# Performance work log

Hardware: AMD Instinct MI355X
Metric: run time of the kernel (lower is better)

The kernel has to match this reference:

```python
import jax, jax.numpy as jnp
import numpy as np
from jax import lax

B, C, H, W = 4, 256, 64, 64
EPS = 1e-5  # BatchNorm eps (eval mode)


def _bn(x, g, b, m, v):
    # eval-mode BatchNorm2d over channel dim
    inv = lax.rsqrt(v + EPS)
    return (x - m[None, :, None, None]) * (g * inv)[None, :, None, None] + b[None, :, None, None]


def _conv1x1(x, w, b):
    # w: [O, I]
    return jnp.einsum('oc,bchw->bohw', w, x) + b[None, :, None, None]


def _conv3x3(x, w, b):
    # w: [O, I, 3, 3], padding 'same'
    y = lax.conv_general_dilated(x, w, (1, 1), 'SAME',
                                 dimension_numbers=('NCHW', 'OIHW', 'NCHW'))
    return y + b[None, :, None, None]


def setup_inputs():
    key = jax.random.key(0)
    ks = jax.random.split(key, 12)
    s = 0.05
    Ch = C // 2
    d = {
        'inputs_0': jax.random.normal(ks[0], (B, C, H, W), jnp.float32),
        'inputs_1': jax.random.normal(ks[1], (B, C, H, W), jnp.float32),
        # 1x1 projections (conv0/conv1/conv2): C -> C/2
        'w_q': jax.random.normal(ks[2], (Ch, C), jnp.float32) * s,
        'b_q': jnp.zeros((Ch,), jnp.float32),
        'w_k': jax.random.normal(ks[3], (Ch, C), jnp.float32) * s,
        'b_k': jnp.zeros((Ch,), jnp.float32),
        'w_v': jax.random.normal(ks[4], (Ch, C), jnp.float32) * s,
        'b_v': jnp.zeros((Ch,), jnp.float32),
        # conv3: C/2 -> C (1x1)
        'w_o': jax.random.normal(ks[5], (C, Ch), jnp.float32) * s,
        'b_o': jnp.zeros((C,), jnp.float32),
        # batch_conv0
        'bn0_g': jnp.ones((C,), jnp.float32), 'bn0_b': jnp.zeros((C,), jnp.float32),
        'bn0_m': jnp.zeros((C,), jnp.float32), 'bn0_v': jnp.ones((C,), jnp.float32),
        # conv_block(2C -> C): conv0 3x3
        'cb_w0': jax.random.normal(ks[6], (C, 2 * C, 3, 3), jnp.float32) * s,
        'cb_b0': jnp.zeros((C,), jnp.float32),
        'cb_bn0_g': jnp.ones((C,), jnp.float32), 'cb_bn0_b': jnp.zeros((C,), jnp.float32),
        'cb_bn0_m': jnp.zeros((C,), jnp.float32), 'cb_bn0_v': jnp.ones((C,), jnp.float32),
        # conv_block conv1 3x3: C -> C
        'cb_w1': jax.random.normal(ks[7], (C, C, 3, 3), jnp.float32) * s,
        'cb_b1': jnp.zeros((C,), jnp.float32),
        'cb_bn1_g': jnp.ones((C,), jnp.float32), 'cb_bn1_b': jnp.zeros((C,), jnp.float32),
        'cb_bn1_m': jnp.zeros((C,), jnp.float32), 'cb_bn1_v': jnp.ones((C,), jnp.float32),
    }
    return d


def reference(inputs_0, inputs_1, w_q, b_q, w_k, b_k, w_v, b_v, w_o, b_o,
              bn0_g, bn0_b, bn0_m, bn0_v,
              cb_w0, cb_b0, cb_bn0_g, cb_bn0_b, cb_bn0_m, cb_bn0_v,
              cb_w1, cb_b1, cb_bn1_g, cb_bn1_b, cb_bn1_m, cb_bn1_v):
    b, c, h, w = inputs_0.shape
    ch = c // 2
    n = h * w
    # 1x1 projections
    x1 = _conv1x1(inputs_0, w_q, b_q).reshape(b, ch, n)   # conv0(inputs_0)
    x2 = _conv1x1(inputs_0, w_k, b_k).reshape(b, ch, n)   # conv1(inputs_0)
    x3 = _conv1x1(inputs_1, w_v, b_v).reshape(b, ch, n)   # conv2(inputs_1)
    # spatial cross-attention: [b, n, n] affinity, contraction over channels
    aff = jnp.einsum('bij,bik->bjk', x2, x3)              # [b, n, n]
    aff = jax.nn.softmax(aff, axis=-2)                    # softmax over dim j (rows)
    x0 = jnp.einsum('bij,bjk->bik', x1, aff)              # [b, ch, n]
    x0 = x0.reshape(b, ch, h, w)
    # output projection + BN + GELU (exact erf gelu, matching torch default)
    x0 = jax.nn.gelu(_bn(_conv1x1(x0, w_o, b_o), bn0_g, bn0_b, bn0_m, bn0_v), approximate=False)
    # conv_block on concat
    y = jnp.concatenate([x0, inputs_0], axis=1)           # [b, 2c, h, w]
    y = jax.nn.gelu(_bn(_conv3x3(y, cb_w0, cb_b0), cb_bn0_g, cb_bn0_b, cb_bn0_m, cb_bn0_v), approximate=False)
    y = jax.nn.gelu(_bn(_conv3x3(y, cb_w1, cb_b1), cb_bn1_g, cb_bn1_b, cb_bn1_m, cb_bn1_v), approximate=False)
    # AdaptiveMaxPool2d((1,1)) == global spatial max, then squeeze -> [b, c]
    out = jnp.max(y + x0, axis=(2, 3))
    return out
```

## Files before the change

### kernel.cpp

```cpp
#include <hip/hip_runtime.h>
#include <math.h>

#define B_ 4
#define C_ 256
#define CH_ 128
#define NN 4096

typedef __bf16 bf16x8 __attribute__((ext_vector_type(8)));
typedef float f32x16 __attribute__((ext_vector_type(16)));
typedef unsigned int u32;

__device__ __forceinline__ float gelu_erf(float x) {
    return 0.5f * x * (1.0f + erff(x * 0.7071067811865476f));
}

__device__ __forceinline__ u32 pkbf(float a, float b) {
    union { __bf16 h[2]; u32 u; } x;
    x.h[0] = (__bf16)a; x.h[1] = (__bf16)b;
    return x.u;
}

__global__ __launch_bounds__(256) void nhwc_cast_kernel(
    const float* __restrict__ src, __bf16* __restrict__ dst,
    int colbase, int rowstride)
{
    __shared__ float Lt[64][65];
    const int t = threadIdx.x;
    const int p0 = blockIdx.x * 64;
    const int c0 = blockIdx.y * 64;
    const int b  = blockIdx.z;
#pragma unroll
    for (int i = 0; i < 16; ++i) {
        int idx = t + i * 256;
        int c = idx >> 6, p = idx & 63;
        Lt[c][p] = src[((size_t)(b * 256 + c0 + c)) * 4096 + p0 + p];
    }
    __syncthreads();
#pragma unroll
    for (int i = 0; i < 16; ++i) {
        int idx = t + i * 256;
        int p = idx >> 6, c = idx & 63;
        dst[((size_t)(b * 4096 + p0 + p)) * rowstride + colbase + c0 + c] = (__bf16)Lt[c][p];
    }
}

__global__ __launch_bounds__(256) void wtrans_kernel(
    const float* __restrict__ w0, const float* __restrict__ w1,
    const float* __restrict__ wq, const float* __restrict__ wk,
    const float* __restrict__ wv, const float* __restrict__ wo,
    __bf16* __restrict__ Wt0, __bf16* __restrict__ Wt1,
    __bf16* __restrict__ wqb, __bf16* __restrict__ wkb,
    __bf16* __restrict__ wvb, __bf16* __restrict__ wob)
{
    int id = blockIdx.x * 256 + threadIdx.x;
    if (id < 131072) {
        int o = id >> 9, ci = id & 511;
        const float* s = w0 + (size_t)id * 9;
        const int chunk = ci >> 4, f = o >> 5;
        const int lane = (o & 31) + 32 * ((ci >> 3) & 1);
        const int j = ci & 7;
#pragma unroll
        for (int k = 0; k < 9; ++k)
            Wt0[((size_t)(chunk * 9 + k) * 8 + f) * 512 + lane * 8 + j] = (__bf16)s[k];
    } else if (id < 196608) {
        int id2 = id - 131072;
        int o = id2 >> 8, ci = id2 & 255;
        const float* s = w1 + (size_t)id2 * 9;
        const int chunk = ci >> 4, f = o >> 5;
        const int lane = (o & 31) + 32 * ((ci >> 3) & 1);
        const int j = ci & 7;
#pragma unroll
        for (int k = 0; k < 9; ++k)
            Wt1[((size_t)(chunk * 9 + k) * 8 + f) * 512 + lane * 8 + j] = (__bf16)s[k];
    } else {
        int id3 = id - 196608;
        int sel = id3 >> 15;
        int k = id3 & 32767;
        const float* s = sel == 0 ? wq : sel == 1 ? wk : sel == 2 ? wv : wo;
        __bf16* d = sel == 0 ? wqb : sel == 1 ? wkb : sel == 2 ? wvb : wob;
        d[k] = (__bf16)s[k];
    }
}

__global__ __launch_bounds__(256) void proj_mfma_kernel(
    const __bf16* __restrict__ Xt0,
    const __bf16* __restrict__ Xin1,
    const __bf16* __restrict__ wqb, const __bf16* __restrict__ wkb,
    const __bf16* __restrict__ wvb,
    const float* __restrict__ bq, const float* __restrict__ bk,
    const float* __restrict__ bv,
    __bf16* __restrict__ Vswz, __bf16* __restrict__ Kswz, __bf16* __restrict__ Qswz)
{
    __shared__ __align__(16) __bf16 Vt[4][64][80];
    __shared__ float biasl[128];

    const int t = threadIdx.x;
    const int which = blockIdx.z % 3;
    const int b = blockIdx.z / 3;
    const int p0 = blockIdx.x * 128;

    const __bf16* W = which == 0 ? wqb : which == 1 ? wkb : wvb;
    const float* bias = which == 0 ? bq : which == 1 ? bk : bv;
    const __bf16* src; int stride, colb;
    if (which == 2) { src = Xin1 + (size_t)b * NN * 256; stride = 256; colb = 0; }
    else            { src = Xt0  + (size_t)b * NN * 512; stride = 512; colb = 256; }

    if (t < 128) biasl[t] = bias[t];
    __syncthreads();

    const int lane = t & 63, w = t >> 6;
    const int l31 = lane & 31, hi = lane >> 5;
    const int wo2 = w >> 1, wp2 = w & 1;
    const int ob = wo2 * 64;
    const int pb = p0 + wp2 * 64;

    f32x16 acc[2][2];
#pragma unroll
    for (int i = 0; i < 2; ++i)
#pragma unroll
        for (int j = 0; j < 2; ++j)
#pragma unroll
            for (int e = 0; e < 16; ++e) acc[i][j][e] = 0.f;

#pragma unroll
    for (int kc = 0; kc < 16; ++kc) {
        bf16x8 a0 = *(const bf16x8*)&W[(size_t)(ob + l31) * 256 + hi * 8 + kc * 16];
        bf16x8 a1 = *(const bf16x8*)&W[(size_t)(ob + 32 + l31) * 256 + hi * 8 + kc * 16];
        bf16x8 b0 = *(const bf16x8*)&src[(size_t)(pb + l31) * stride + colb + hi * 8 + kc * 16];
        bf16x8 b1 = *(const bf16x8*)&src[(size_t)(pb + 32 + l31) * stride + colb + hi * 8 + kc * 16];
        acc[0][0] = __builtin_amdgcn_mfma_f32_32x32x16_bf16(a0, b0, acc[0][0], 0, 0, 0);
        acc[0][1] = __builtin_amdgcn_mfma_f32_32x32x16_bf16(a0, b1, acc[0][1], 0, 0, 0);
        acc[1][0] = __builtin_amdgcn_mfma_f32_32x32x16_bf16(a1, b0, acc[1][0], 0, 0, 0);
        acc[1][1] = __builtin_amdgcn_mfma_f32_32x32x16_bf16(a1, b1, acc[1][1], 0, 0, 0);
    }

    if (which) {
        __bf16* dst = (which == 1 ? Kswz : Qswz) + (size_t)b * NN * CH_;
#pragma unroll
        for (int mi = 0; mi < 2; ++mi)
#pragma unroll
            for (int nx = 0; nx < 2; ++nx) {
                const int tile = (pb >> 5) + nx;
#pragma unroll
                for (int q4 = 0; q4 < 4; ++q4) {
                    const int ic = (ob >> 4) + mi * 2 + (q4 >> 1);
                    const int og = ob + mi * 32 + q4 * 8 + hi * 4;
                    __bf16 pk[4];
#pragma unroll
                    for (int j = 0; j < 4; ++j)
                        pk[j] = (__bf16)(acc[mi][nx][q4 * 4 + j] + biasl[og + j]);
                    const size_t el = ((size_t)(tile * 8 + ic) * 64
                                       + l31 + 32 * (q4 & 1)) * 8 + hi * 4;
                    *(uint2*)&dst[el] = *(const uint2*)pk;
                }
            }
    } else {
#pragma unroll
        for (int mi = 0; mi < 2; ++mi)
#pragma unroll
            for (int nx = 0; nx < 2; ++nx) {
                const int ploc = nx * 32 + l31;
#pragma unroll
                for (int q4 = 0; q4 < 4; ++q4) {
                    const int oloc = mi * 32 + q4 * 8 + hi * 4;
#pragma unroll
                    for (int j = 0; j < 4; ++j)
                        Vt[w][oloc + j][ploc] =
                            (__bf16)(acc[mi][nx][q4 * 4 + j] + biasl[ob + oloc + j]);
                }
            }
        __syncthreads();
        __bf16* dst = Vswz + (size_t)b * NN * CH_;
#pragma unroll
        for (int s = 0; s < 8; ++s) {
            const int tl = s >> 2, jc = (s >> 1) & 1, il = s & 1;
            const int tile_g = (pb >> 5) + tl;
            const int icf_g = (ob >> 5) + il;
            const int i_loc = il * 32 + l31;
            const int kk = tl * 32 + jc * 16 + hi * 8;
            uint4 v = *(const uint4*)&Vt[w][i_loc][kk];
            const size_t el = ((size_t)((tile_g * 2 + jc) * 4 + icf_g) * 64 + lane) * 8;
            *(uint4*)&dst[el] = v;
        }
    }
}

__global__ __launch_bounds__(256, 4) void attn_mfma_kernel(
    const __bf16* __restrict__ Qswz, const __bf16* __restrict__ Kswz,
    const __bf16* __restrict__ Vswz,
    __bf16* __restrict__ Opart, float* __restrict__ Mpart, float* __restrict__ Lpart)
{
    __shared__ __bf16 Op[4][128][34];
    __shared__ float Ml[4][32], Ll[4][32];

    const int t = threadIdx.x;
    const int lane = t & 63;
    const int w = t >> 6;
    const int l31 = lane & 31;
    const int hi = lane >> 5;

    const int bid = blockIdx.x;
    const int xcd = bid & 7;
    const int b = xcd >> 1;
    const int local = bid >> 3;
    const int qt = (xcd & 1) * 64 + (local & 63);
    const int half = local >> 6;
    const int q0 = qt * 32;

    const __bf16* Qs = Qswz + (size_t)b * NN * CH_ + (size_t)qt * 4096 + lane * 8;
    bf16x8 qf[8];
#pragma unroll
    for (int ic = 0; ic < 8; ++ic) qf[ic] = *(const bf16x8*)(Qs + ic * 512);

    const __bf16* Ks = Kswz + (size_t)b * NN * CH_ + lane * 8;
    const __bf16* Vs = Vswz + (size_t)b * NN * CH_ + lane * 8;

    f32x16 oacc[4];
#pragma unroll
    for (int i = 0; i < 4; ++i)
#pragma unroll
        for (int e = 0; e < 16; ++e) oacc[i][e] = 0.f;

    float m = -3e38f, lsum = 0.f;
    const int tbase = half * 64 + w * 16;

    for (int jt = 0; jt < 16; ++jt) {
        const int tile = tbase + jt;
        f32x16 s;
#pragma unroll
        for (int e = 0; e < 16; ++e) s[e] = 0.f;
        const __bf16* Kt = Ks + (size_t)tile * 4096;
#pragma unroll
        for (int ic = 0; ic < 8; ++ic) {
            bf16x8 kf = *(const bf16x8*)(Kt + ic * 512);
            s = __builtin_amdgcn_mfma_f32_32x32x16_bf16(kf, qf[ic], s, 0, 0, 0);
        }
        float t8[8];
#pragma unroll
        for (int e = 0; e < 8; ++e) t8[e] = fmaxf(s[e], s[e + 8]);
#pragma unroll
        for (int e = 0; e < 4; ++e) t8[e] = fmaxf(t8[e], t8[e + 4]);
        t8[0] = fmaxf(t8[0], t8[2]); t8[1] = fmaxf(t8[1], t8[3]);
        float mu = fmaxf(t8[0], t8[1]);
        const float pm = fmaxf(mu, __shfl_xor(mu, 32));
        if (!__all(pm <= m + 8.f)) {
            const float mn = fmaxf(m, pm);
            const float al = __expf(m - mn);
            m = mn;
            lsum *= al;
#pragma unroll
            for (int i = 0; i < 4; ++i)
#pragma unroll
                for (int e = 0; e < 16; ++e) oacc[i][e] *= al;
        }
#pragma unroll
        for (int e = 0; e < 16; ++e) s[e] = __expf(s[e] - m);
        float s8[8];
#pragma unroll
        for (int e = 0; e < 8; ++e) s8[e] = s[e] + s[e + 8];
#pragma unroll
        for (int e = 0; e < 4; ++e) s8[e] += s8[e + 4];
        s8[0] += s8[2]; s8[1] += s8[3];
        float su = s8[0] + s8[1];
        lsum += su + __shfl_xor(su, 32);

        const __bf16* Vt = Vs + (size_t)tile * 4096;
        {
            u32 w0 = pkbf(s[0], s[1]), w1 = pkbf(s[2], s[3]);
            u32 w2 = pkbf(s[4], s[5]), w3 = pkbf(s[6], s[7]);
            asm("v_permlane32_swap_b32 %0, %1" : "+v"(w0), "+v"(w2));
            asm("v_permlane32_swap_b32 %0, %1" : "+v"(w1), "+v"(w3));
            union { u32 u4[4]; bf16x8 v; } pB;
            pB.u4[0] = w0; pB.u4[1] = w1; pB.u4[2] = w2; pB.u4[3] = w3;
#pragma unroll
            for (int icf = 0; icf < 4; ++icf) {
                bf16x8 vf = *(const bf16x8*)(Vt + icf * 512);
                oacc[icf] = __builtin_amdgcn_mfma_f32_32x32x16_bf16(vf, pB.v, oacc[icf], 0, 0, 0);
            }
        }
        {
            u32 w0 = pkbf(s[8], s[9]), w1 = pkbf(s[10], s[11]);
            u32 w2 = pkbf(s[12], s[13]), w3 = pkbf(s[14], s[15]);
            asm("v_permlane32_swap_b32 %0, %1" : "+v"(w0), "+v"(w2));
            asm("v_permlane32_swap_b32 %0, %1" : "+v"(w1), "+v"(w3));
            union { u32 u4[4]; bf16x8 v; } pB;
            pB.u4[0] = w0; pB.u4[1] = w1; pB.u4[2] = w2; pB.u4[3] = w3;
#pragma unroll
            for (int icf = 0; icf < 4; ++icf) {
                bf16x8 vf = *(const bf16x8*)(Vt + 2048 + icf * 512);
                oacc[icf] = __builtin_amdgcn_mfma_f32_32x32x16_bf16(vf, pB.v, oacc[icf], 0, 0, 0);
            }
        }
    }

#pragma unroll
    for (int icf = 0; icf < 4; ++icf)
#pragma unroll
        for (int q = 0; q < 16; ++q) {
            const int row = icf * 32 + (q & 3) + 8 * (q >> 2) + 4 * hi;
            Op[w][row][l31] = (__bf16)oacc[icf][q];
        }
    if (hi == 0) { Ml[w][l31] = m; Ll[w][l31] = lsum; }
    __syncthreads();
    {
        const int q = t & 31;
        const int i0g = (t >> 5) * 16;
        const float m0 = Ml[0][q], m1 = Ml[1][q], m2 = Ml[2][q], m3 = Ml[3][q];
        const float ms = fmaxf(fmaxf(m0, m1), fmaxf(m2, m3));
        const float a0 = __expf(m0 - ms), a1 = __expf(m1 - ms);
        const float a2 = __expf(m2 - ms), a3 = __expf(m3 - ms);
        const float den = a0 * Ll[0][q] + a1 * Ll[1][q] + a2 * Ll[2][q] + a3 * Ll[3][q];
        union { __bf16 h[16]; uint4 u4[2]; } pk;
#pragma unroll
        for (int ii = 0; ii < 16; ++ii) {
            const int i = i0g + ii;
            pk.h[ii] = (__bf16)(a0 * (float)Op[0][i][q] + a1 * (float)Op[1][i][q]
                              + a2 * (float)Op[2][i][q] + a3 * (float)Op[3][i][q]);
        }
        const size_t base = ((size_t)((half * 4 + b) * NN) + q0 + q) * CH_ + i0g;
        *(uint4*)&Opart[base] = pk.u4[0];
        *(uint4*)&Opart[base + 8] = pk.u4[1];
        if (t < 32) {
            Mpart[(size_t)(half * 4 + b) * NN + q0 + q] = ms;
            Lpart[(size_t)(half * 4 + b) * NN + q0 + q] = den;
        }
    }
}

__global__ __launch_bounds__(256) void attn_merge_kernel(
    const __bf16* __restrict__ Opart, const float* __restrict__ Mpart,
    const float* __restrict__ Lpart, __bf16* __restrict__ x0)
{
    const int id = blockIdx.x * 256 + threadIdx.x;
    const int qg = id >> 2;
    const int i0 = (id & 3) * 32;
    const int b = qg >> 12, q = qg & 4095;
    const size_t idx0 = (size_t)b * NN + q;
    const size_t idx1 = (size_t)(4 + b) * NN + q;
    const float m0 = Mpart[idx0], m1 = Mpart[idx1];
    const float ms = fmaxf(m0, m1);
    const float a0 = __expf(m0 - ms), a1 = __expf(m1 - ms);
    const float inv = 1.f / (a0 * Lpart[idx0] + a1 * Lpart[idx1]);
    const __bf16* O0 = &Opart[idx0 * CH_ + i0];
    const __bf16* O1 = &Opart[idx1 * CH_ + i0];
    union { __bf16 h[32]; uint4 u4[4]; } ov;
#pragma unroll
    for (int ii = 0; ii < 32; ++ii)
        ov.h[ii] = (__bf16)((a0 * (float)O0[ii] + a1 * (float)O1[ii]) * inv);
    uint4* dst = (uint4*)&x0[((size_t)b * NN + q) * CH_ + i0];
#pragma unroll
    for (int s = 0; s < 4; ++s) dst[s] = ov.u4[s];
}

__global__ __launch_bounds__(256) void convo_mfma_kernel(
    const __bf16* __restrict__ x0, const __bf16* __restrict__ wob,
    const float* __restrict__ bo,
    const float* __restrict__ g, const float* __restrict__ bb,
    const float* __restrict__ mm, const float* __restrict__ vv,
    __bf16* __restrict__ Xt0)
{
    __shared__ float scb[128], shb[128], bsb[128];
    const int t = threadIdx.x;
    const int p0 = blockIdx.x * 128;
    const int o0 = blockIdx.y * 128;
    const int b = blockIdx.z;
    if (t < 128) {
        const int o = o0 + t;
        const float sc = g[o] * rsqrtf(vv[o] + 1e-5f);
        scb[t] = sc; shb[t] = bb[o] - mm[o] * sc; bsb[t] = bo[o];
    }
    __syncthreads();

    const int lane = t & 63, w = t >> 6;
    const int l31 = lane & 31, hi = lane >> 5;
    const int wo2 = w >> 1, wp2 = w & 1;
    const int ob = o0 + wo2 * 64;
    const int pb = p0 + wp2 * 64;

    f32x16 acc[2][2];
#pragma unroll
    for (int i = 0; i < 2; ++i)
#pragma unroll
        for (int j = 0; j < 2; ++j)
#pragma unroll
            for (int e = 0; e < 16; ++e) acc[i][j][e] = 0.f;

#pragma unroll
    for (int kc = 0; kc < 8; ++kc) {
        bf16x8 a0 = *(const bf16x8*)&wob[(size_t)(ob + l31) * 128 + hi * 8 + kc * 16];
        bf16x8 a1 = *(const bf16x8*)&wob[(size_t)(ob + 32 + l31) * 128 + hi * 8 + kc * 16];
        bf16x8 b0 = *(const bf16x8*)&x0[((size_t)(b * NN) + pb + l31) * 128 + hi * 8 + kc * 16];
        bf16x8 b1 = *(const bf16x8*)&x0[((size_t)(b * NN) + pb + 32 + l31) * 128 + hi * 8 + kc * 16];
        acc[0][0] = __builtin_amdgcn_mfma_f32_32x32x16_bf16(a0, b0, acc[0][0], 0, 0, 0);
        acc[0][1] = __builtin_amdgcn_mfma_f32_32x32x16_bf16(a0, b1, acc[0][1], 0, 0, 0);
        acc[1][0] = __builtin_amdgcn_mfma_f32_32x32x16_bf16(a1, b0, acc[1][0], 0, 0, 0);
        acc[1][1] = __builtin_amdgcn_mfma_f32_32x32x16_bf16(a1, b1, acc[1][1], 0, 0, 0);
    }

#pragma unroll
    for (int mi = 0; mi < 2; ++mi)
#pragma unroll
        for (int nx = 0; nx < 2; ++nx) {
            const int p = pb + nx * 32 + l31;
            const size_t rowbase = ((size_t)(b * NN) + p) * 512 + o0;
#pragma unroll
            for (int q4 = 0; q4 < 4; ++q4) {
                const int ol = wo2 * 64 + mi * 32 + q4 * 8 + hi * 4;
                __bf16 pk[4];
#pragma unroll
                for (int j = 0; j < 4; ++j) {
                    float v = acc[mi][nx][q4 * 4 + j] + bsb[ol + j];
                    v = v * scb[ol + j] + shb[ol + j];
                    pk[j] = (__bf16)gelu_erf(v);
                }
                *(uint2*)&Xt0[rowbase + ol] = *(const uint2*)pk;
            }
        }
}

template<int IC>
__global__ __launch_bounds__(128) void conv3x3_mfma_kernel(
    const __bf16* __restrict__ Xsrc,
    const __bf16* __restrict__ Wf,
    const float* __restrict__ bias, const float* __restrict__ bng,
    const float* __restrict__ bnb, const float* __restrict__ bnm,
    const float* __restrict__ bnv,
    __bf16* __restrict__ out)
{
    constexpr int NC = IC / 16;
    __shared__ __align__(16) char Tl[2][6336];
    __shared__ float scb[64], shb[64], bsb[64];

    const int t = threadIdx.x;
    const int bid = blockIdx.x;
    const int xcd = bid & 7, local = bid >> 3;
    const int combo = xcd * 2 + (local >> 6);
    const int y0 = local & 63;
    const int m = combo & 3, b = combo >> 2;
    const int o0 = m * 64;

    if (t < 64) {
        const int o = o0 + t;
        const float sc = bng[o] * rsqrtf(bnv[o] + 1e-5f);
        scb[t] = sc; shb[t] = bnb[o] - bnm[o] * sc; bsb[t] = bias[o];
    }

    const int lane = t & 63, w = t >> 6;
    const int l31 = lane & 31, hi = lane >> 5;

    uint4 ireg[3];

    auto loadI = [&](int c0) {
#pragma unroll
        for (int s = 0; s < 3; ++s) {
            int u = t + s * 128;
            int g = u & 1, x = (u >> 1) & 63, r = u >> 7;
            int yy = y0 - 1 + r;
            if (yy >= 0 && yy < 64)
                ireg[s] = *(const uint4*)&Xsrc[((size_t)(b * 4096 + yy * 64 + x)) * IC + c0 + g * 8];
            else
                ireg[s] = make_uint4(0u, 0u, 0u, 0u);
        }
    };
    auto writeI = [&](char* dst) {
#pragma unroll
        for (int s = 0; s < 3; ++s) {
            int u = t + s * 128;
            int g = u & 1, x = (u >> 1) & 63, r = u >> 7;
            int xh = x + 1;
            int byte = r * 2112 + ((xh * 32 + g * 16) ^ ((xh & 7) << 4));
            *(uint4*)(dst + byte) = ireg[s];
        }
        if (t < 12) {
            int g = t & 1, side = (t >> 1) & 1, r = t >> 2;
            int xh = side ? 65 : 0;
            int byte = r * 2112 + ((xh * 32 + g * 16) ^ ((xh & 7) << 4));
            *(uint4*)(dst + byte) = make_uint4(0u, 0u, 0u, 0u);
        }
    };

    const __bf16* Wb = Wf + ((size_t)(m * 2) * 64 + lane) * 8;
    bf16x8 wA[9][2];
    auto loadA = [&](int c) {
#pragma unroll
        for (int k9 = 0; k9 < 9; ++k9) {
            const __bf16* wp = Wb + (size_t)(c * 9 + k9) * 4096;
            wA[k9][0] = *(const bf16x8*)(wp);
            wA[k9][1] = *(const bf16x8*)(wp + 512);
        }
    };

    f32x16 acc[2];
#pragma unroll
    for (int i = 0; i < 2; ++i)
#pragma unroll
        for (int e = 0; e < 16; ++e) acc[i][e] = 0.f;

    int Boff[3];
#pragma unroll
    for (int dx = 0; dx < 3; ++dx) {
        int xh = w * 32 + l31 + dx;
        Boff[dx] = (xh * 32 + hi * 16) ^ ((xh & 7) << 4);
    }

    auto compute = [&](const char* Tb) {
#pragma unroll
        for (int k9 = 0; k9 < 9; ++k9) {
            const int dy = k9 / 3, dx = k9 % 3;
            bf16x8 bv = *(const bf16x8*)(Tb + dy * 2112 + Boff[dx]);
            acc[0] = __builtin_amdgcn_mfma_f32_32x32x16_bf16(wA[k9][0], bv, acc[0], 0, 0, 0);
            acc[1] = __builtin_amdgcn_mfma_f32_32x32x16_bf16(wA[k9][1], bv, acc[1], 0, 0, 0);
        }
    };

    loadI(0); loadA(0);
    writeI(Tl[0]);
    __syncthreads();
    for (int c = 0; c < NC; ++c) {
        const int cur = c & 1;
        if (c + 1 < NC) loadI((c + 1) * 16);
        compute(Tl[cur]);
        if (c + 1 < NC) loadA(c + 1);
        __syncthreads();
        if (c + 1 < NC) writeI(Tl[cur ^ 1]);
        __syncthreads();
    }

    {
        const int p = y0 * 64 + w * 32 + l31;
        const size_t rowbase = ((size_t)(b * 4096 + p)) * 256 + o0;
#pragma unroll
        for (int mi = 0; mi < 2; ++mi)
#pragma unroll
            for (int q = 0; q < 4; ++q) {
                const int obase = mi * 32 + q * 8 + hi * 4;
                __bf16 pk[4];
#pragma unroll
                for (int j = 0; j < 4; ++j) {
                    float v = acc[mi][q * 4 + j] + bsb[obase + j];
                    v = v * scb[obase + j] + shb[obase + j];
                    pk[j] = (__bf16)gelu_erf(v);
                }
                *(uint2*)&out[rowbase + obase] = *(const uint2*)pk;
            }
    }
}

__global__ __launch_bounds__(256) void maxpart_kernel(
    const __bf16* __restrict__ y1, const __bf16* __restrict__ xt0,
    float* __restrict__ part)
{
    const int o = threadIdx.x;
    const int chunk = blockIdx.x & 63;
    const int b = blockIdx.x >> 6;
    float mx = -1e30f;
    for (int pp = 0; pp < 64; ++pp) {
        int p = chunk * 64 + pp;
        float a = (float)y1[((size_t)(b * 4096 + p)) * 256 + o];
        float c = (float)xt0[((size_t)(b * 4096 + p)) * 512 + o];
        mx = fmaxf(mx, a + c);
    }
    part[((size_t)(b * 64 + chunk)) * 256 + o] = mx;
}

__global__ __launch_bounds__(256) void maxfin_kernel(
    const float* __restrict__ part, float* __restrict__ out)
{
    const int o = threadIdx.x;
    const int b = blockIdx.x;
    float mx = -1e30f;
    for (int c = 0; c < 64; ++c)
        mx = fmaxf(mx, part[((size_t)(b * 64 + c)) * 256 + o]);
    out[b * 256 + o] = mx;
}

extern "C" void kernel_launch(void* const* d_in, const int* in_sizes, int n_in,
                              void* d_out, int out_size, void* d_ws, size_t ws_size,
                              hipStream_t stream)
{
    const float* in0  = (const float*)d_in[0];
    const float* in1  = (const float*)d_in[1];
    const float* w_q  = (const float*)d_in[2];
    const float* b_q  = (const float*)d_in[3];
    const float* w_k  = (const float*)d_in[4];
    const float* b_k  = (const float*)d_in[5];
    const float* w_v  = (const float*)d_in[6];
    const float* b_v  = (const float*)d_in[7];
    const float* w_o  = (const float*)d_in[8];
    const float* b_o  = (const float*)d_in[9];
    const float* bn0g = (const float*)d_in[10];
    const float* bn0b = (const float*)d_in[11];
    const float* bn0m = (const float*)d_in[12];
    const float* bn0v = (const float*)d_in[13];
    const float* cbw0 = (const float*)d_in[14];
    const float* cbb0 = (const float*)d_in[15];
    const float* cb0g = (const float*)d_in[16];
    const float* cb0b = (const float*)d_in[17];
    const float* cb0m = (const float*)d_in[18];
    const float* cb0v = (const float*)d_in[19];
    const float* cbw1 = (const float*)d_in[20];
    const float* cbb1 = (const float*)d_in[21];
    const float* cb1g = (const float*)d_in[22];
    const float* cb1b = (const float*)d_in[23];
    const float* cb1m = (const float*)d_in[24];
    const float* cb1v = (const float*)d_in[25];

    char* wsb = (char*)d_ws;
    const size_t MB = 1u << 20;
    __bf16* Xt0  = (__bf16*)(wsb);
    __bf16* Xin1 = (__bf16*)(wsb + 16 * MB);
    __bf16* Opart= (__bf16*)(wsb + 16 * MB);
    __bf16* Qswz = (__bf16*)(wsb + 24 * MB);
    __bf16* x0   = (__bf16*)(wsb + 24 * MB);
    __bf16* Kswz = (__bf16*)(wsb + 28 * MB);
    __bf16* y0   = (__bf16*)(wsb + 24 * MB);
    __bf16* Vswz = (__bf16*)(wsb + 32 * MB);
    __bf16* y1   = (__bf16*)(wsb + 32 * MB);
    __bf16* wqb  = (__bf16*)(wsb + 40 * MB);
    __bf16* wkb  = (__bf16*)(wsb + 40 * MB + 65536);
    __bf16* wvb  = (__bf16*)(wsb + 40 * MB + 2 * 65536);
    __bf16* wob  = (__bf16*)(wsb + 40 * MB + 3 * 65536);
    __bf16* Wt0  = (__bf16*)(wsb + 40 * MB + 4 * 65536);
    __bf16* Wt1  = (__bf16*)(wsb + 40 * MB + 4 * 65536 + 2359296);
    float*  Mpart= (float*)(wsb + 44 * MB);
    float*  Lpart= (float*)(wsb + 44 * MB + 131072);
    float*  part = (float*)(wsb + 44 * MB + 2 * 131072);
    float* outp = (float*)d_out;

    nhwc_cast_kernel<<<dim3(64, 4, 4), 256, 0, stream>>>(in0, Xt0, 256, 512);
    nhwc_cast_kernel<<<dim3(64, 4, 4), 256, 0, stream>>>(in1, Xin1, 0, 256);
    wtrans_kernel<<<1280, 256, 0, stream>>>(cbw0, cbw1, w_q, w_k, w_v, w_o,
                                            Wt0, Wt1, wqb, wkb, wvb, wob);
    proj_mfma_kernel<<<dim3(32, 1, 12), 256, 0, stream>>>(
        Xt0, Xin1, wqb, wkb, wvb, b_q, b_k, b_v, Vswz, Kswz, Qswz);
    attn_mfma_kernel<<<1024, 256, 0, stream>>>(Qswz, Kswz, Vswz, Opart, Mpart, Lpart);
    attn_merge_kernel<<<256, 256, 0, stream>>>(Opart, Mpart, Lpart, x0);
    convo_mfma_kernel<<<dim3(32, 2, 4), 256, 0, stream>>>(
        x0, wob, b_o, bn0g, bn0b, bn0m, bn0v, Xt0);
    conv3x3_mfma_kernel<512><<<1024, 128, 0, stream>>>(Xt0, Wt0, cbb0, cb0g, cb0b, cb0m, cb0v, y0);
    conv3x3_mfma_kernel<256><<<1024, 128, 0, stream>>>(y0, Wt1, cbb1, cb1g, cb1b, cb1m, cb1v, y1);
    maxpart_kernel<<<256, 256, 0, stream>>>(y1, Xt0, part);
    maxfin_kernel<<<4, 256, 0, stream>>>(part, outp);
}
```

Baseline: 251.3 us.

## Double conv3x3 channel chunk, drop one barrier, prefetch weights per tap

The 3x3 conv MFMA kernel now handles 32 input channels per main-loop iteration instead of 16. The shared input tile doubles in size and uses a new XOR slot swizzle. Each iteration needs only one __syncthreads instead of two. The next chunk's weights are loaded tap by tap, right after each tap's MFMAs use the current registers, so weight loads overlap the matrix work. This amortizes barriers and loop overhead over more MFMAs, but roughly doubles the weight and input staging registers and the LDS footprint, which can lower occupancy.

New measurement: 253.8 us. About the same (+1.0%).

```diff
diff --git a/kernel.cpp b/kernel.cpp
--- a/kernel.cpp
+++ b/kernel.cpp
@@ -427,8 +427,8 @@
     const float* __restrict__ bnv,
     __bf16* __restrict__ out)
 {
-    constexpr int NC = IC / 16;
-    __shared__ __align__(16) char Tl[2][6336];
+    constexpr int NC2 = IC / 32;
+    __shared__ __align__(16) char Tl[2][12672];
     __shared__ float scb[64], shb[64], bsb[64];
 
     const int t = threadIdx.x;
@@ -448,46 +448,46 @@
     const int lane = t & 63, w = t >> 6;
     const int l31 = lane & 31, hi = lane >> 5;
 
-    uint4 ireg[3];
+    uint4 ireg[6];
 
     auto loadI = [&](int c0) {
 #pragma unroll
-        for (int s = 0; s < 3; ++s) {
+        for (int s = 0; s < 6; ++s) {
             int u = t + s * 128;
-            int g = u & 1, x = (u >> 1) & 63, r = u >> 7;
+            int sl = u & 3, x = (u >> 2) & 63, r = u >> 8;
             int yy = y0 - 1 + r;
             if (yy >= 0 && yy < 64)
-                ireg[s] = *(const uint4*)&Xsrc[((size_t)(b * 4096 + yy * 64 + x)) * IC + c0 + g * 8];
+                ireg[s] = *(const uint4*)&Xsrc[((size_t)(b * 4096 + yy * 64 + x)) * IC + c0 + sl * 8];
             else
                 ireg[s] = make_uint4(0u, 0u, 0u, 0u);
         }
     };
     auto writeI = [&](char* dst) {
 #pragma unroll
-        for (int s = 0; s < 3; ++s) {
+        for (int s = 0; s < 6; ++s) {
             int u = t + s * 128;
-            int g = u & 1, x = (u >> 1) & 63, r = u >> 7;
+            int sl = u & 3, x = (u >> 2) & 63, r = u >> 8;
             int xh = x + 1;
-            int byte = r * 2112 + ((xh * 32 + g * 16) ^ ((xh & 7) << 4));
-            *(uint4*)(dst + byte) = ireg[s];
-        }
-        if (t < 12) {
-            int g = t & 1, side = (t >> 1) & 1, r = t >> 2;
+            int slot = (xh * 4 + sl) ^ (xh & 7);
+            *(uint4*)(dst + r * 4224 + slot * 16) = ireg[s];
+        }
+        if (t < 24) {
+            int sl = t & 3, side = (t >> 2) & 1, r = t >> 3;
             int xh = side ? 65 : 0;
-            int byte = r * 2112 + ((xh * 32 + g * 16) ^ ((xh & 7) << 4));
-            *(uint4*)(dst + byte) = make_uint4(0u, 0u, 0u, 0u);
+            int slot = (xh * 4 + sl) ^ (xh & 7);
+            *(uint4*)(dst + r * 4224 + slot * 16) = make_uint4(0u, 0u, 0u, 0u);
         }
     };
 
     const __bf16* Wb = Wf + ((size_t)(m * 2) * 64 + lane) * 8;
-    bf16x8 wA[9][2];
-    auto loadA = [&](int c) {
-#pragma unroll
-        for (int k9 = 0; k9 < 9; ++k9) {
-            const __bf16* wp = Wb + (size_t)(c * 9 + k9) * 4096;
-            wA[k9][0] = *(const bf16x8*)(wp);
-            wA[k9][1] = *(const bf16x8*)(wp + 512);
-        }
+    bf16x8 wA[9][2][2];
+    auto loadAk = [&](int cc, int k9) {
+        const __bf16* wp0 = Wb + (size_t)((2 * cc) * 9 + k9) * 4096;
+        const __bf16* wp1 = Wb + (size_t)((2 * cc + 1) * 9 + k9) * 4096;
+        wA[k9][0][0] = *(const bf16x8*)(wp0);
+        wA[k9][0][1] = *(const bf16x8*)(wp0 + 512);
+        wA[k9][1][0] = *(const bf16x8*)(wp1);
+        wA[k9][1][1] = *(const bf16x8*)(wp1 + 512);
     };
 
     f32x16 acc[2];
@@ -496,33 +496,41 @@
 #pragma unroll
         for (int e = 0; e < 16; ++e) acc[i][e] = 0.f;
 
-    int Boff[3];
+    int Boff[3][2];
 #pragma unroll
     for (int dx = 0; dx < 3; ++dx) {
         int xh = w * 32 + l31 + dx;
-        Boff[dx] = (xh * 32 + hi * 16) ^ ((xh & 7) << 4);
-    }
-
-    auto compute = [&](const char* Tb) {
+#pragma unroll
+        for (int g = 0; g < 2; ++g)
+            Boff[dx][g] = ((xh * 4 + g * 2 + hi) ^ (xh & 7)) * 16;
+    }
+
+    auto computePF = [&](const char* Tb, int ccNext) {
 #pragma unroll
         for (int k9 = 0; k9 < 9; ++k9) {
             const int dy = k9 / 3, dx = k9 % 3;
-            bf16x8 bv = *(const bf16x8*)(Tb + dy * 2112 + Boff[dx]);
-            acc[0] = __builtin_amdgcn_mfma_f32_32x32x16_bf16(wA[k9][0], bv, acc[0], 0, 0, 0);
-            acc[1] = __builtin_amdgcn_mfma_f32_32x32x16_bf16(wA[k9][1], bv, acc[1], 0, 0, 0);
+            const char* Trow = Tb + dy * 4224;
+            bf16x8 bv0 = *(const bf16x8*)(Trow + Boff[dx][0]);
+            bf16x8 bv1 = *(const bf16x8*)(Trow + Boff[dx][1]);
+            acc[0] = __builtin_amdgcn_mfma_f32_32x32x16_bf16(wA[k9][0][0], bv0, acc[0], 0, 0, 0);
+            acc[1] = __builtin_amdgcn_mfma_f32_32x32x16_bf16(wA[k9][0][1], bv0, acc[1], 0, 0, 0);
+            acc[0] = __builtin_amdgcn_mfma_f32_32x32x16_bf16(wA[k9][1][0], bv1, acc[0], 0, 0, 0);
+            acc[1] = __builtin_amdgcn_mfma_f32_32x32x16_bf16(wA[k9][1][1], bv1, acc[1], 0, 0, 0);
+            loadAk(ccNext, k9);
         }
     };
 
-    loadI(0); loadA(0);
+    loadI(0);
+#pragma unroll
+    for (int k9 = 0; k9 < 9; ++k9) loadAk(0, k9);
     writeI(Tl[0]);
     __syncthreads();
-    for (int c = 0; c < NC; ++c) {
+    for (int c = 0; c < NC2; ++c) {
         const int cur = c & 1;
-        if (c + 1 < NC) loadI((c + 1) * 16);
-        compute(Tl[cur]);
-        if (c + 1 < NC) loadA(c + 1);
-        __syncthreads();
-        if (c + 1 < NC) writeI(Tl[cur ^ 1]);
+        const int cn = (c + 1 < NC2) ? c + 1 : c;
+        loadI(cn * 32);
+        computePF(Tl[cur], cn);
+        writeI(Tl[cur ^ 1]);
         __syncthreads();
     }
 
```

## Remap conv3x3 blocks per XCD by batch and vectorize max-pool partial reduction

Applied to the files above, without the earlier changes.

The conv3x3 block-to-work mapping is changed so each XCD handles one batch and one half of the rows across all output-channel groups. The goal is for blocks on the same XCD to share input tiles in their L2 rather than spreading one batch over several XCDs. The maxpart kernel now loads 8 bf16 values per 16-byte load, with each thread covering 8 channels over 8 pixels, and combines the partial maxima through shared memory. This replaces scalar 2-byte loads and adds a barrier plus a shared-memory pass.

Result: faster. 243.7 us (-3.0%).

```diff
diff --git a/kernel.cpp b/kernel.cpp
--- a/kernel.cpp
+++ b/kernel.cpp
@@ -434,9 +434,9 @@
     const int t = threadIdx.x;
     const int bid = blockIdx.x;
     const int xcd = bid & 7, local = bid >> 3;
-    const int combo = xcd * 2 + (local >> 6);
-    const int y0 = local & 63;
-    const int m = combo & 3, b = combo >> 2;
+    const int b = xcd >> 1, yhi = xcd & 1;
+    const int y0 = yhi * 32 + (local & 31);
+    const int m = local >> 5;
     const int o0 = m * 64;
 
     if (t < 64) {
@@ -550,17 +550,35 @@
     const __bf16* __restrict__ y1, const __bf16* __restrict__ xt0,
     float* __restrict__ part)
 {
-    const int o = threadIdx.x;
+    __shared__ float sm[8][32][8];
+    const int t = threadIdx.x;
     const int chunk = blockIdx.x & 63;
     const int b = blockIdx.x >> 6;
-    float mx = -1e30f;
-    for (int pp = 0; pp < 64; ++pp) {
-        int p = chunk * 64 + pp;
-        float a = (float)y1[((size_t)(b * 4096 + p)) * 256 + o];
-        float c = (float)xt0[((size_t)(b * 4096 + p)) * 512 + o];
-        mx = fmaxf(mx, a + c);
-    }
-    part[((size_t)(b * 64 + chunk)) * 256 + o] = mx;
+    const int pp = t >> 5;
+    const int og = t & 31;
+
+    float mx[8];
+#pragma unroll
+    for (int j = 0; j < 8; ++j) mx[j] = -1e30f;
+    for (int i = 0; i < 8; ++i) {
+        const int p = chunk * 64 + pp * 8 + i;
+        union { uint4 u; __bf16 h[8]; } a, c;
+        a.u = *(const uint4*)&y1[((size_t)(b * 4096 + p)) * 256 + og * 8];
+        c.u = *(const uint4*)&xt0[((size_t)(b * 4096 + p)) * 512 + og * 8];
+#pragma unroll
+        for (int j = 0; j < 8; ++j)
+            mx[j] = fmaxf(mx[j], (float)a.h[j] + (float)c.h[j]);
+    }
+#pragma unroll
+    for (int j = 0; j < 8; ++j) sm[pp][og][j] = mx[j];
+    __syncthreads();
+    {
+        const int og2 = t >> 3, j = t & 7;
+        float m = sm[0][og2][j];
+#pragma unroll
+        for (int p2 = 1; p2 < 8; ++p2) m = fmaxf(m, sm[p2][og2][j]);
+        part[((size_t)(b * 64 + chunk)) * 256 + og2 * 8 + j] = m;
+    }
 }
 
 __global__ __launch_bounds__(256) void maxfin_kernel(
```

## Fuse residual-add and max-pool partials into second conv3x3, merge cast launches

Applied to the files above, without the earlier changes.

The second 3x3 conv epilogue now adds the x0 residual and reduces a per-row spatial max with shuffles and shared memory, writing partial maxima directly. This removes the y1 write/read round trip and the separate maxpart kernel. The two input cast kernels are merged into one launch. The block-to-tile mapping is changed so each XCD handles one batch and half the rows with all channel tiles. One of the two barriers per K-step is dropped by writing the next input tile before a single sync.

Measured after the change: 239.1 us. 4.8% less time.

```diff
diff --git a/kernel.cpp b/kernel.cpp
--- a/kernel.cpp
+++ b/kernel.cpp
@@ -20,15 +20,19 @@
     return x.u;
 }
 
-__global__ __launch_bounds__(256) void nhwc_cast_kernel(
-    const float* __restrict__ src, __bf16* __restrict__ dst,
-    int colbase, int rowstride)
+__global__ __launch_bounds__(256) void nhwc_cast2_kernel(
+    const float* __restrict__ in0, const float* __restrict__ in1,
+    __bf16* __restrict__ Xt0, __bf16* __restrict__ Xin1)
 {
     __shared__ float Lt[64][65];
     const int t = threadIdx.x;
     const int p0 = blockIdx.x * 64;
     const int c0 = blockIdx.y * 64;
-    const int b  = blockIdx.z;
+    const int z = blockIdx.z;
+    const int b = z & 3;
+    const float* src; __bf16* dst; int colbase, rowstride;
+    if (z < 4) { src = in0; dst = Xt0; colbase = 256; rowstride = 512; }
+    else       { src = in1; dst = Xin1; colbase = 0;  rowstride = 256; }
 #pragma unroll
     for (int i = 0; i < 16; ++i) {
         int idx = t + i * 256;
@@ -418,25 +422,28 @@
         }
 }
 
-template<int IC>
+template<int IC, bool FUSEMAX>
 __global__ __launch_bounds__(128) void conv3x3_mfma_kernel(
     const __bf16* __restrict__ Xsrc,
     const __bf16* __restrict__ Wf,
     const float* __restrict__ bias, const float* __restrict__ bng,
     const float* __restrict__ bnb, const float* __restrict__ bnm,
     const float* __restrict__ bnv,
-    __bf16* __restrict__ out)
+    __bf16* __restrict__ out,
+    const __bf16* __restrict__ Xg,
+    float* __restrict__ part)
 {
     constexpr int NC = IC / 16;
     __shared__ __align__(16) char Tl[2][6336];
     __shared__ float scb[64], shb[64], bsb[64];
+    __shared__ float red[2][64];
 
     const int t = threadIdx.x;
     const int bid = blockIdx.x;
     const int xcd = bid & 7, local = bid >> 3;
-    const int combo = xcd * 2 + (local >> 6);
-    const int y0 = local & 63;
-    const int m = combo & 3, b = combo >> 2;
+    const int b = xcd >> 1, yhi = xcd & 1;
+    const int y0 = yhi * 32 + (local & 31);
+    const int m = local >> 5;
     const int o0 = m * 64;
 
     if (t < 64) {
@@ -520,14 +527,12 @@
         const int cur = c & 1;
         if (c + 1 < NC) loadI((c + 1) * 16);
         compute(Tl[cur]);
-        if (c + 1 < NC) loadA(c + 1);
+        if (c + 1 < NC) { loadA(c + 1); writeI(Tl[cur ^ 1]); }
         __syncthreads();
-        if (c + 1 < NC) writeI(Tl[cur ^ 1]);
-        __syncthreads();
-    }
-
-    {
-        const int p = y0 * 64 + w * 32 + l31;
+    }
+
+    const int p = y0 * 64 + w * 32 + l31;
+    if constexpr (!FUSEMAX) {
         const size_t rowbase = ((size_t)(b * 4096 + p)) * 256 + o0;
 #pragma unroll
         for (int mi = 0; mi < 2; ++mi)
@@ -543,24 +548,42 @@
                 }
                 *(uint2*)&out[rowbase + obase] = *(const uint2*)pk;
             }
-    }
-}
-
-__global__ __launch_bounds__(256) void maxpart_kernel(
-    const __bf16* __restrict__ y1, const __bf16* __restrict__ xt0,
-    float* __restrict__ part)
-{
-    const int o = threadIdx.x;
-    const int chunk = blockIdx.x & 63;
-    const int b = blockIdx.x >> 6;
-    float mx = -1e30f;
-    for (int pp = 0; pp < 64; ++pp) {
-        int p = chunk * 64 + pp;
-        float a = (float)y1[((size_t)(b * 4096 + p)) * 256 + o];
-        float c = (float)xt0[((size_t)(b * 4096 + p)) * 512 + o];
-        mx = fmaxf(mx, a + c);
-    }
-    part[((size_t)(b * 64 + chunk)) * 256 + o] = mx;
+    } else {
+        const size_t xbase = ((size_t)(b * 4096 + p)) * 512 + o0;
+#pragma unroll
+        for (int mi = 0; mi < 2; ++mi)
+#pragma unroll
+            for (int q = 0; q < 4; ++q) {
+                const int obase = mi * 32 + q * 8 + hi * 4;
+                union { uint2 u; __bf16 h[4]; } xg;
+                xg.u = *(const uint2*)&Xg[xbase + obase];
+#pragma unroll
+                for (int j = 0; j < 4; ++j) {
+                    float v = acc[mi][q * 4 + j] + bsb[obase + j];
+                    v = v * scb[obase + j] + shb[obase + j];
+                    acc[mi][q * 4 + j] = gelu_erf(v) + (float)xg.h[j];
+                }
+            }
+#pragma unroll
+        for (int off = 1; off < 32; off <<= 1)
+#pragma unroll
+            for (int mi = 0; mi < 2; ++mi)
+#pragma unroll
+                for (int e = 0; e < 16; ++e)
+                    acc[mi][e] = fmaxf(acc[mi][e], __shfl_xor(acc[mi][e], off));
+        if (l31 == 0) {
+#pragma unroll
+            for (int mi = 0; mi < 2; ++mi)
+#pragma unroll
+                for (int q = 0; q < 4; ++q)
+#pragma unroll
+                    for (int j = 0; j < 4; ++j)
+                        red[w][mi * 32 + q * 8 + hi * 4 + j] = acc[mi][q * 4 + j];
+        }
+        __syncthreads();
+        if (t < 64)
+            part[((size_t)(b * 64 + y0)) * 256 + o0 + t] = fmaxf(red[0][t], red[1][t]);
+    }
 }
 
 __global__ __launch_bounds__(256) void maxfin_kernel(
@@ -615,7 +638,6 @@
     __bf16* Kswz = (__bf16*)(wsb + 28 * MB);
     __bf16* y0   = (__bf16*)(wsb + 24 * MB);
     __bf16* Vswz = (__bf16*)(wsb + 32 * MB);
-    __bf16* y1   = (__bf16*)(wsb + 32 * MB);
     __bf16* wqb  = (__bf16*)(wsb + 40 * MB);
     __bf16* wkb  = (__bf16*)(wsb + 40 * MB + 65536);
     __bf16* wvb  = (__bf16*)(wsb + 40 * MB + 2 * 65536);
@@ -627,8 +649,7 @@
     float*  part = (float*)(wsb + 44 * MB + 2 * 131072);
     float* outp = (float*)d_out;
 
-    nhwc_cast_kernel<<<dim3(64, 4, 4), 256, 0, stream>>>(in0, Xt0, 256, 512);
-    nhwc_cast_kernel<<<dim3(64, 4, 4), 256, 0, stream>>>(in1, Xin1, 0, 256);
+    nhwc_cast2_kernel<<<dim3(64, 4, 8), 256, 0, stream>>>(in0, in1, Xt0, Xin1);
     wtrans_kernel<<<1280, 256, 0, stream>>>(cbw0, cbw1, w_q, w_k, w_v, w_o,
                                             Wt0, Wt1, wqb, wkb, wvb, wob);
     proj_mfma_kernel<<<dim3(32, 1, 12), 256, 0, stream>>>(
@@ -637,8 +658,9 @@
     attn_merge_kernel<<<256, 256, 0, stream>>>(Opart, Mpart, Lpart, x0);
     convo_mfma_kernel<<<dim3(32, 2, 4), 256, 0, stream>>>(
         x0, wob, b_o, bn0g, bn0b, bn0m, bn0v, Xt0);
-    conv3x3_mfma_kernel<512><<<1024, 128, 0, stream>>>(Xt0, Wt0, cbb0, cb0g, cb0b, cb0m, cb0v, y0);
-    conv3x3_mfma_kernel<256><<<1024, 128, 0, stream>>>(y0, Wt1, cbb1, cb1g, cb1b, cb1m, cb1v, y1);
-    maxpart_kernel<<<256, 256, 0, stream>>>(y1, Xt0, part);
+    conv3x3_mfma_kernel<512, false><<<1024, 128, 0, stream>>>(
+        Xt0, Wt0, cbb0, cb0g, cb0b, cb0m, cb0v, y0, nullptr, nullptr);
+    conv3x3_mfma_kernel<256, true><<<1024, 128, 0, stream>>>(
+        y0, Wt1, cbb1, cb1g, cb1b, cb1m, cb1v, nullptr, Xt0, part);
     maxfin_kernel<<<4, 256, 0, stream>>>(part, outp);
 }
```
